# Performance work log

Hardware: AMD Instinct MI355X
Metric: run time of the kernel (lower is better)

## Reference

```python
import jax, jax.numpy as jnp
import numpy as np

B, N, H, KRATE = 128, 400, 128, 0.2
EPS = 1e-9


def setup_inputs() -> dict:
    key = jax.random.key(0)
    ks = jax.random.split(key, 16)
    # correlation-like input: symmetric, values in (-1,1), unit diagonal
    x = jax.random.normal(ks[0], (B, N, N), dtype=jnp.float32)
    x = jnp.tanh(0.3 * x)
    x = 0.5 * (x + x.transpose(0, 2, 1))
    eye = jnp.eye(N, dtype=jnp.float32)
    x = x * (1.0 - eye) + eye

    def lin(k, fan_in, shape):
        return jax.random.normal(k, shape, dtype=jnp.float32) / np.sqrt(fan_in).astype(np.float32)

    return {
        "x": x,
        "slength": jnp.full((B,), 100, dtype=jnp.int32),
        # AE denoiser (num_of_node=N, hidden=H)
        "enc1_w": lin(ks[1], N, (N, H)), "enc1_b": jnp.zeros((H,), jnp.float32),
        "enc2_w": lin(ks[2], N, (N, H)), "enc2_b": jnp.zeros((H,), jnp.float32),
        "dec2_w": lin(ks[3], H, (H, N)), "dec2_b": jnp.zeros((N,), jnp.float32),
        "dec1_w": lin(ks[4], H, (H, N)), "dec1_b": jnp.zeros((N,), jnp.float32),
        # GCN predictor
        "gcn1_w": lin(ks[5], N, (N, H)), "gcn1_b": jnp.zeros((H,), jnp.float32),
        "gcn2_w": lin(ks[6], H, (H, H)), "gcn2_b": jnp.zeros((H,), jnp.float32),
        # classification head Linear(128 -> 2)
        "fc_w": lin(ks[7], H, (H, 2)), "fc_b": jnp.zeros((2,), jnp.float32),
    }


def reference(x, slength, enc1_w, enc1_b, enc2_w, enc2_b, dec2_w, dec2_b,
              dec1_w, dec1_b, gcn1_w, gcn1_b, gcn2_w, gcn2_b, fc_w, fc_b):
    eye = jnp.eye(N, dtype=x.dtype)

    # fisher transform + normalize by [0,0] entry
    xf = 0.5 * jnp.log((1.0 + x + EPS) / (1.0 - x + EPS))
    xf = xf / xf[:, 0, 0][:, None, None]

    # --- DA / AE denoiser: deltax = AE(xf), symmetrized ---
    out1 = jax.nn.relu(jnp.einsum('bij,jh->bih', xf, enc1_w) + enc1_b).transpose(0, 2, 1)  # [B,H,N]
    out2 = jax.nn.relu(jnp.einsum('bhn,nk->bhk', out1, enc2_w) + enc2_b)                   # [B,H,H]
    out2 = jax.nn.relu(jnp.einsum('bhk,kn->bhn', out2, dec2_w) + dec2_b + out1)            # [B,H,N]
    out2 = out2.transpose(0, 2, 1)                                                         # [B,N,H]
    delta = jnp.einsum('bnh,hm->bnm', out2, dec1_w) + dec1_b                               # [B,N,N]
    delta = 0.5 * (delta + delta.transpose(0, 2, 1))
    x2 = xf + delta * (1.0 - eye)

    # --- predictor on detached x2 ---
    xp = jax.lax.stop_gradient(x2)

    # topk sparsification at rate 0.2 over flattened NxN per sample
    k = int(N * N * KRATE)
    flat = xp.reshape(B, N * N)
    _, idx = jax.lax.top_k(flat, k)
    mask = jnp.zeros((B, N * N), xp.dtype).at[jnp.arange(B)[:, None], idx].set(1.0)
    A = xp * mask.reshape(B, N, N)

    # GCN norm (PyG gcn_norm with add_remaining_self_loops, fill=1)
    diag = jnp.diagonal(A, axis1=1, axis2=2)
    A = A + eye[None] * jnp.where(diag == 0.0, 1.0, 0.0)[:, :, None]
    deg = A.sum(axis=1)                      # scatter of edge weight on col index
    dinv = deg ** -0.5
    dinv = jnp.where(jnp.isinf(dinv), 0.0, dinv)
    An = dinv[:, :, None] * A * dinv[:, None, :]  # An[b,i,j] = dinv[i]*A[i,j]*dinv[j]

    # GCNConv1 -> ReLU -> GCNConv2 (aggregate onto col/target index)
    h = jax.nn.relu(jnp.einsum('bij,bif->bjf', An, xp @ gcn1_w) + gcn1_b)  # [B,N,H]
    h = jnp.einsum('bij,bif->bjf', An, h @ gcn2_w) + gcn2_b                # [B,N,H]

    pooled = h.mean(axis=1)                  # mean over nodes -> [B,H]
    out = jax.nn.relu(pooled) @ fc_w + fc_b  # [B,2]
    return out
```

## Files before the change

### kernel.cpp

```cpp
#include <hip/hip_runtime.h>
#include <hip/hip_bf16.h>
#include <math.h>

#define BATCH 128
#define NNODE 400
#define HID   128
#define NN    (NNODE*NNODE)
#define KSEL  32000
#define EQCAP 1024
#define EPSF  1e-9f
#define TSPLIT 8
#define SEG   (NN / TSPLIT)
#define NT    7
#define KC400 14
#define FRAGS (KC400*4096)
#define PLA   57344

__device__ __forceinline__ unsigned tokey(float f) {
  unsigned u = __float_as_uint(f);
  return (u & 0x80000000u) ? ~u : (u | 0x80000000u);
}

__device__ __forceinline__ short f2bf(float f) {
  unsigned u = __float_as_uint(f);
  u += 0x7fffu + ((u >> 16) & 1u);
  return (short)(u >> 16);
}
__device__ __forceinline__ float bf2f(short s) {
  return __uint_as_float(((unsigned)(unsigned short)s) << 16);
}

__device__ __forceinline__ float xfhw(float xv, float cmul) {
  float la = __builtin_amdgcn_logf(1.0f + xv + EPSF);
  float lb = __builtin_amdgcn_logf(1.0f - xv + EPSF);
  return (la - lb) * cmul;
}

typedef __attribute__((ext_vector_type(8))) short s8v;
typedef __attribute__((ext_vector_type(4))) short s4v;
typedef __attribute__((ext_vector_type(4))) float f4v;

#define BK 16
#define LP 68

template<bool AT, bool BIAS, bool RES, bool RELU, bool TS>
__global__ void __launch_bounds__(256) gemm64(
    const float* __restrict__ A, long sA, int lda,
    const float* __restrict__ B, long sB, int ldb,
    const float* __restrict__ bias,
    const float* __restrict__ Res, long sRes,
    float* __restrict__ C, long sC, int ldc,
    int M, int Nc, int K)
{
  __shared__ float As[BK][LP];
  __shared__ float Bs[BK][LP];
  const int bz = blockIdx.z;
  A += (size_t)bz * sA;
  B += (size_t)bz * sB;
  C += (size_t)bz * sC;
  const float* Rp = RES ? (Res + (size_t)bz * sRes) : nullptr;

  const int n0 = blockIdx.x * 64;
  const int m0 = blockIdx.y * 64;
  const int tid = threadIdx.x;
  const int tx = tid & 15, ty = tid >> 4;
  const bool edgeM = (m0 + 64 > M);
  const bool edgeN = (n0 + 64 > Nc);

  float acc[4][4];
#pragma unroll
  for (int i = 0; i < 4; ++i)
#pragma unroll
    for (int j = 0; j < 4; ++j) acc[i][j] = 0.f;

  for (int k0 = 0; k0 < K; k0 += BK) {
    if (!AT) {
      const int m = tid & 63, g = tid >> 6;
      if (!edgeM) {
        const float4 v = *(const float4*)(A + (size_t)(m0 + m) * lda + k0 + 4 * g);
        As[4 * g + 0][m] = v.x; As[4 * g + 1][m] = v.y;
        As[4 * g + 2][m] = v.z; As[4 * g + 3][m] = v.w;
      } else {
        const int gm = m0 + m;
        const bool ok = gm < M;
#pragma unroll
        for (int j = 0; j < 4; ++j)
          As[4 * g + j][m] = ok ? A[(size_t)gm * lda + k0 + 4 * g + j] : 0.f;
      }
    } else {
      const int k = tid >> 4, mg = tid & 15;
      if (!edgeM) {
        const float4 v = *(const float4*)(A + (size_t)(k0 + k) * lda + m0 + 4 * mg);
        *(float4*)&As[k][4 * mg] = v;
      } else {
#pragma unroll
        for (int j = 0; j < 4; ++j) {
          const int gm = m0 + 4 * mg + j;
          As[k][4 * mg + j] = (gm < M) ? A[(size_t)(k0 + k) * lda + gm] : 0.f;
        }
      }
    }
    {
      const int k = tid >> 4, ng = tid & 15;
      if (!edgeN) {
        const float4 v = *(const float4*)(B + (size_t)(k0 + k) * ldb + n0 + 4 * ng);
        *(float4*)&Bs[k][4 * ng] = v;
      } else {
#pragma unroll
        for (int j = 0; j < 4; ++j) {
          const int gn = n0 + 4 * ng + j;
          Bs[k][4 * ng + j] = (gn < Nc) ? B[(size_t)(k0 + k) * ldb + gn] : 0.f;
        }
      }
    }
    __syncthreads();
#pragma unroll
    for (int kk = 0; kk < BK; ++kk) {
      const float4 a = *(const float4*)&As[kk][ty << 2];
      const float4 b = *(const float4*)&Bs[kk][tx << 2];
      const float av[4] = {a.x, a.y, a.z, a.w};
      const float bv[4] = {b.x, b.y, b.z, b.w};
#pragma unroll
      for (int i = 0; i < 4; ++i)
#pragma unroll
        for (int j = 0; j < 4; ++j) acc[i][j] += av[i] * bv[j];
    }
    __syncthreads();
  }

#pragma unroll
  for (int i = 0; i < 4; ++i) {
    const int m = m0 + (ty << 2) + i;
    if (m >= M) continue;
#pragma unroll
    for (int j = 0; j < 4; ++j) {
      const int n = n0 + (tx << 2) + j;
      if (n >= Nc) continue;
      float v = acc[i][j];
      if (BIAS) v += bias[n];
      const size_t loc = TS ? ((size_t)n * ldc + m) : ((size_t)m * ldc + n);
      if (RES) v += Rp[loc];
      if (RELU) v = fmaxf(v, 0.f);
      C[loc] = v;
    }
  }
}

__global__ void bsplit5(
    const float* __restrict__ gcn1_w, const float* __restrict__ gcn2_w,
    const float* __restrict__ enc1_w, const float* __restrict__ enc2_w,
    const float* __restrict__ dec1_w,
    short* __restrict__ w1frag, short* __restrict__ w2frag,
    short* __restrict__ e1frag, short* __restrict__ e2frag,
    short* __restrict__ dfrag) {
  const float* W; short* out; int K, Kpad, N, Npad;
  switch (blockIdx.y) {
    case 0: W = gcn1_w; out = w1frag; K = NNODE; Kpad = 448; N = HID;   Npad = 128; break;
    case 1: W = gcn2_w; out = w2frag; K = HID;   Kpad = 128; N = HID;   Npad = 128; break;
    case 2: W = enc1_w; out = e1frag; K = NNODE; Kpad = 448; N = HID;   Npad = 128; break;
    case 3: W = enc2_w; out = e2frag; K = NNODE; Kpad = 448; N = HID;   Npad = 128; break;
    default: W = dec1_w; out = dfrag; K = HID;   Kpad = 128; N = NNODE; Npad = 448; break;
  }
  int t = blockIdx.x * 256 + threadIdx.x;
  if (t >= Kpad * Npad) return;
  int k = t / Npad, n = t - k * Npad;
  float v = (k < K && n < N) ? W[(size_t)k * N + n] : 0.f;
  short hi = f2bf(v);
  short lo = f2bf(v - bf2f(hi));
  int ntiles = Npad >> 4;
  size_t idx = (((size_t)(k >> 5) * ntiles + (n >> 4)) * 64
                + (((k >> 3) & 3) * 16 + (n & 15))) * 8 + (k & 7);
  size_t PL = (size_t)(Kpad >> 5) * ntiles * 512;
  out[idx] = hi;
  out[PL + idx] = lo;
}

template<bool AT, bool FRAG, bool BIAS, bool RELU, bool SCL, bool TS, bool XF,
         bool MASK, bool DSCL>
__global__ void __launch_bounds__(256) mfgemm(
    const float* __restrict__ A, long sA, int lda,
    const short* __restrict__ Bf, long sB, int kc,
    const float* __restrict__ bias,
    const float* __restrict__ scl,
    float* __restrict__ Cf, long sCf, int ldc,
    short* __restrict__ Cfrag, long sCfrag, int okc,
    const float* __restrict__ denomp, float* __restrict__ xfout,
    const unsigned* __restrict__ taup, float* __restrict__ Aout,
    float* __restrict__ degp, int* __restrict__ eqcntp,
    int* __restrict__ eqidxp, const float* __restrict__ dsclp,
    int M, int K)
{
  __shared__ float As[64][68];
  __shared__ float cs[MASK ? NNODE : 1];
  const int bz = blockIdx.y;
  A += (size_t)bz * sA;
  Bf += (size_t)bz * sB;
  if (SCL) scl += (size_t)bz * NNODE;
  if (!FRAG) Cf += (size_t)bz * sCf;
  else       Cfrag += (size_t)bz * sCfrag;
  if (XF) xfout += (size_t)bz * sA;
  const float cmul = XF ? (0.34657359027997264f / denomp[bz]) : 0.f;
  const unsigned tk = MASK ? taup[bz] : 0u;
  if (MASK) { Aout += (size_t)bz * NN; degp += (size_t)bz * NNODE;
              eqcntp += bz; eqidxp += (size_t)bz * EQCAP; }
  if (DSCL) dsclp += (size_t)bz * NNODE;

  const int tid = threadIdx.x;
  const int lane = tid & 63, wave = tid >> 6;
  const int wqm = wave >> 1, wqn = wave & 1;
  const int quad = lane >> 4, l15 = lane & 15;
  const int m0 = blockIdx.x * 64;

  if (MASK) {
    for (int i = tid; i < NNODE; i += 256) cs[i] = 0.f;
    __syncthreads();
  }

  f4v acc[2][4];
#pragma unroll
  for (int i = 0; i < 2; ++i)
#pragma unroll
    for (int j = 0; j < 4; ++j) acc[i][j] = (f4v){0.f, 0.f, 0.f, 0.f};

  const int nstage = (K + 63) >> 6;
  for (int st = 0; st < nstage; ++st) {
    const int k0 = st << 6;
    if (st) __syncthreads();
    if (!AT) {
      const int mrow = tid >> 4;
      const int k4 = (tid & 15) << 2;
#pragma unroll
      for (int u = 0; u < 4; ++u) {
        const int m = mrow + (u << 4);
        const int gm = m0 + m, gk = k0 + k4;
        float4 v = {0.f, 0.f, 0.f, 0.f};
        if (gm < M) {
          if (gk + 4 <= K) {
            float4 xv = *(const float4*)(A + (size_t)gm * lda + gk);
            if (XF) {
              v.x = xfhw(xv.x, cmul);
              v.y = xfhw(xv.y, cmul);
              v.z = xfhw(xv.z, cmul);
              v.w = xfhw(xv.w, cmul);
              *(float4*)(xfout + (size_t)gm * lda + gk) = v;
            } else v = xv;
            if (MASK) {
              float4 av;
              float* pa = (float*)&av;
              const float* px = (const float*)&v;
#pragma unroll
              for (int j = 0; j < 4; ++j) {
                const unsigned key = tokey(px[j]);
                float a = (key > tk) ? px[j] : 0.f;
                if (key == tk) {
                  int p = atomicAdd(eqcntp, 1);
                  if (p < EQCAP) eqidxp[p] = gm * NNODE + gk + j;
                }
                if (a != 0.f) atomicAdd(&cs[gk + j], a);
                pa[j] = a;
              }
              *(float4*)(Aout + (size_t)gm * NNODE + gk) = av;
            }
          } else {
            float* pv = (float*)&v;
#pragma unroll
            for (int j = 0; j < 4; ++j)
              if (gk + j < K) {
                float xv = A[(size_t)gm * lda + gk + j];
                if (XF) {
                  pv[j] = xfhw(xv, cmul);
                  xfout[(size_t)gm * lda + gk + j] = pv[j];
                } else pv[j] = xv;
                if (MASK) {
                  const unsigned key = tokey(pv[j]);
                  float a = (key > tk) ? pv[j] : 0.f;
                  if (key == tk) {
                    int p = atomicAdd(eqcntp, 1);
                    if (p < EQCAP) eqidxp[p] = gm * NNODE + gk + j;
                  }
                  if (a != 0.f) atomicAdd(&cs[gk + j], a);
                  Aout[(size_t)gm * NNODE + gk + j] = a;
                }
              }
          }
        }
        *(float4*)&As[m][k4] = v;
      }
    } else {
      const int kk = tid >> 4;
      const int m4 = (tid & 15) << 2;
#pragma unroll
      for (int u = 0; u < 4; ++u) {
        const int gk = k0 + kk + (u << 4);
        float4 v = {0.f, 0.f, 0.f, 0.f};
        if (gk < K) {
          const float ds = DSCL ? dsclp[gk] : 1.f;
          if (m0 + m4 + 4 <= M) {
            v = *(const float4*)(A + (size_t)gk * lda + m0 + m4);
            if (DSCL) { v.x *= ds; v.y *= ds; v.z *= ds; v.w *= ds; }
          } else {
            float* pv = (float*)&v;
#pragma unroll
            for (int j = 0; j < 4; ++j)
              if (m0 + m4 + j < M) {
                float t = A[(size_t)gk * lda + m0 + m4 + j];
                pv[j] = DSCL ? t * ds : t;
              }
          }
        }
        As[m4 + 0][kk + (u << 4)] = v.x;
        As[m4 + 1][kk + (u << 4)] = v.y;
        As[m4 + 2][kk + (u << 4)] = v.z;
        As[m4 + 3][kk + (u << 4)] = v.w;
      }
    }
    __syncthreads();

#pragma unroll
    for (int c2 = 0; c2 < 2; ++c2) {
      const int c = (st << 1) + c2;
      s8v bhi[4], blo[4];
#pragma unroll
      for (int nt = 0; nt < 4; ++nt) {
        const int ntg = (wqn << 2) + nt;
        const size_t off = (((size_t)c * 8 + ntg) * 64 + lane) * 8;
        bhi[nt] = *(const s8v*)(Bf + off);
        blo[nt] = *(const s8v*)(Bf + (size_t)kc * 4096 + off);
      }
#pragma unroll
      for (int mt = 0; mt < 2; ++mt) {
        const int row = (wqm << 5) + (mt << 4) + l15;
        const int kof = (c2 << 5) + (quad << 3);
        const f4v a0 = *(const f4v*)&As[row][kof];
        const f4v a1 = *(const f4v*)&As[row][kof + 4];
        s8v ah, al;
#pragma unroll
        for (int j = 0; j < 4; ++j) {
          short h0 = f2bf(a0[j]); ah[j] = h0; al[j] = f2bf(a0[j] - bf2f(h0));
          short h1 = f2bf(a1[j]); ah[j + 4] = h1; al[j + 4] = f2bf(a1[j] - bf2f(h1));
        }
#pragma unroll
        for (int nt = 0; nt < 4; ++nt) {
          acc[mt][nt] = __builtin_amdgcn_mfma_f32_16x16x32_bf16(ah, bhi[nt], acc[mt][nt], 0, 0, 0);
          acc[mt][nt] = __builtin_amdgcn_mfma_f32_16x16x32_bf16(ah, blo[nt], acc[mt][nt], 0, 0, 0);
          acc[mt][nt] = __builtin_amdgcn_mfma_f32_16x16x32_bf16(al, bhi[nt], acc[mt][nt], 0, 0, 0);
        }
      }
    }
  }

  if (MASK) {
    __syncthreads();
    for (int j = tid; j < NNODE; j += 256) {
      const float s = cs[j];
      if (s != 0.f) atomicAdd(&degp[j], s);
    }
  }

  if (TS) {
    for (int nh = 0; nh < 2; ++nh) {
      __syncthreads();
      if (wqn == nh) {
#pragma unroll
        for (int mt = 0; mt < 2; ++mt)
#pragma unroll
          for (int nt = 0; nt < 4; ++nt) {
            const int tn = (nt << 4) + l15;
            const int n  = (wqn << 6) + tn;
            const int mc = (wqm << 5) + (mt << 4) + (quad << 2);
            const f4v a = acc[mt][nt];
#pragma unroll
            for (int reg = 0; reg < 4; ++reg) {
              float v = a[reg];
              if (SCL) v *= scl[m0 + mc + reg];
              if (BIAS) v += bias[n];
              if (RELU) v = fmaxf(v, 0.f);
              As[tn][mc + reg] = v;
            }
          }
      }
      __syncthreads();
      const int row = tid >> 2, cq = tid & 3;
#pragma unroll
      for (int u = 0; u < 4; ++u) {
        const int col = (cq + (u << 2)) << 2;
        if (m0 + col + 4 <= M) {
          const float4 v = *(const float4*)&As[row][col];
          *(float4*)(Cf + (size_t)((nh << 6) + row) * ldc + m0 + col) = v;
        }
      }
    }
    return;
  }

#pragma unroll
  for (int mt = 0; mt < 2; ++mt) {
    const int mb = m0 + (wqm << 5) + (mt << 4) + (quad << 2);
#pragma unroll
    for (int nt = 0; nt < 4; ++nt) {
      const int n = (wqn << 6) + (nt << 4) + l15;
      const f4v a = acc[mt][nt];
      if (!FRAG) {
#pragma unroll
        for (int reg = 0; reg < 4; ++reg) {
          const int m = mb + reg;
          if (m < M) {
            float v = a[reg];
            if (SCL) v *= scl[m];
            if (BIAS) v += bias[n];
            if (RELU) v = fmaxf(v, 0.f);
            Cf[(size_t)m * ldc + n] = v;
          }
        }
      } else {
        s4v h4, l4;
#pragma unroll
        for (int reg = 0; reg < 4; ++reg) {
          const int m = mb + reg;
          float v = (m < M) ? (SCL ? a[reg] * scl[m] : a[reg]) : 0.f;
          short hh = f2bf(v);
          h4[reg] = hh; l4[reg] = f2bf(v - bf2f(hh));
        }
        const int chunkT = mb >> 5, quadT = (mb >> 3) & 3, jT0 = mb & 7;
        const size_t off = (((size_t)chunkT * 8 + (wqn << 2) + nt) * 64
                            + quadT * 16 + l15) * 8 + jT0;
        *(s4v*)(Cfrag + off) = h4;
        *(s4v*)(Cfrag + (size_t)okc * 4096 + off) = l4;
      }
    }
  }
}

__global__ void __launch_bounds__(256) g4mf(
    const float* __restrict__ o1,
    const short* __restrict__ wfrag,
    const float* __restrict__ bias,
    float* __restrict__ xf,
    unsigned* __restrict__ ghist)
{
  __shared__ float D2[64][68];
  __shared__ unsigned hist[2048];
  const int b = blockIdx.y;
  int p = blockIdx.x, bi = 0;
  while (p >= NT - bi) { p -= NT - bi; ++bi; }
  const int bj = bi + p;
  const int I0 = bi * 64, J0 = bj * 64;
  const bool diag = (bi == bj);

  o1 += (size_t)b * HID * NNODE;
  xf += (size_t)b * NN;
  unsigned* gh = ghist + (size_t)b * 4096;

  const int tid = threadIdx.x;
  const int lane = tid & 63, wave = tid >> 6;
  const int wq = wave & 1;
  const bool d1 = wave < 2;
  const int Bt = (d1 ? bj : bi) * 4;
  const int quad = lane >> 4, l15 = lane & 15;
  const int M0 = d1 ? I0 : J0;

  for (int i = tid; i < 2048; i += 256) hist[i] = 0u;

  f4v acc[2][4];
#pragma unroll
  for (int i = 0; i < 2; ++i)
#pragma unroll
    for (int j = 0; j < 4; ++j) acc[i][j] = (f4v){0.f, 0.f, 0.f, 0.f};

  const int gm0 = M0 + (wq << 5) + l15;

  for (int c = 0; c < 4; ++c) {
    const int k0 = c << 5;
    s8v bhi[4], blo[4];
#pragma unroll
    for (int nt = 0; nt < 4; ++nt) {
      const int ntg = Bt + nt;
      const size_t off = (((size_t)c * 28 + ntg) * 64 + lane) * 8;
      bhi[nt] = *(const s8v*)(wfrag + off);
      blo[nt] = *(const s8v*)(wfrag + PLA + off);
    }
#pragma unroll
    for (int mt = 0; mt < 2; ++mt) {
      const int gm = gm0 + (mt << 4);
      float av[8];
      if (gm < NNODE) {
        const float* cp = o1 + (size_t)(k0 + (quad << 3)) * NNODE + gm;
#pragma unroll
        for (int j = 0; j < 8; ++j) av[j] = cp[(size_t)j * NNODE];
      } else {
#pragma unroll
        for (int j = 0; j < 8; ++j) av[j] = 0.f;
      }
      s8v ah, al;
#pragma unroll
      for (int j = 0; j < 8; ++j) {
        short h = f2bf(av[j]); ah[j] = h; al[j] = f2bf(av[j] - bf2f(h));
      }
#pragma unroll
      for (int nt = 0; nt < 4; ++nt) {
        acc[mt][nt] = __builtin_amdgcn_mfma_f32_16x16x32_bf16(ah, bhi[nt], acc[mt][nt], 0, 0, 0);
        acc[mt][nt] = __builtin_amdgcn_mfma_f32_16x16x32_bf16(ah, blo[nt], acc[mt][nt], 0, 0, 0);
        acc[mt][nt] = __builtin_amdgcn_mfma_f32_16x16x32_bf16(al, bhi[nt], acc[mt][nt], 0, 0, 0);
      }
    }
  }

  if (!d1) {
#pragma unroll
    for (int mt = 0; mt < 2; ++mt) {
      const int mb = (wq << 5) + (mt << 4) + (quad << 2);
#pragma unroll
      for (int nt = 0; nt < 4; ++nt) {
        const int nn = (nt << 4) + l15;
        const f4v a = acc[mt][nt];
#pragma unroll
        for (int reg = 0; reg < 4; ++reg) D2[mb + reg][nn] = a[reg];
      }
    }
  }
  __syncthreads();

  if (d1) {
    const unsigned w = diag ? 1u : 2u;
#pragma unroll
    for (int mt = 0; mt < 2; ++mt) {
      const int a0 = (wq << 5) + (mt << 4) + (quad << 2);
#pragma unroll
      for (int nt = 0; nt < 4; ++nt) {
        const int nn = (nt << 4) + l15;
        const int gj = J0 + nn;
        const f4v d1v = acc[mt][nt];
        const f4v d2t = *(const f4v*)&D2[nn][a0];
        f4v vv;
#pragma unroll
        for (int reg = 0; reg < 4; ++reg) {
          const int gi = I0 + a0 + reg;
          float v = 0.f;
          if (gi < NNODE && gj < NNODE) {
            v = xf[(size_t)gi * NNODE + gj];
            if (gi != gj)
              v += 0.5f * (d1v[reg] + d2t[reg] + bias[gj] + bias[gi]);
            const unsigned bin = tokey(v) >> 20;
            atomicAdd(&hist[bin >> 1], w << ((bin & 1) << 4));
          }
          vv[reg] = v;
        }
#pragma unroll
        for (int reg = 0; reg < 4; ++reg) {
          const int gi = I0 + a0 + reg;
          if (gi < NNODE && gj < NNODE) xf[(size_t)gi * NNODE + gj] = vv[reg];
        }
        if (!diag && gj < NNODE && (I0 + a0 + 4 <= NNODE)) {
          *(float4*)(xf + (size_t)gj * NNODE + I0 + a0) = *(float4*)&vv;
        }
      }
    }
  }
  __syncthreads();
  for (int i = tid; i < 2048; i += 256) {
    const unsigned v = hist[i];
    const unsigned lo = v & 0xFFFFu, hi = v >> 16;
    if (lo) atomicAdd(&gh[2 * i], lo);
    if (hi) atomicAdd(&gh[2 * i + 1], hi);
  }
}

__global__ void tzd(const float* __restrict__ x, unsigned* __restrict__ ghist,
                    unsigned* __restrict__ sprefix, int* __restrict__ sk,
                    int* __restrict__ eqcnt, float* __restrict__ deg,
                    float* __restrict__ denom, unsigned* __restrict__ ccnt2) {
  int t = blockIdx.x * 256 + threadIdx.x;
  if (t < BATCH * 4096) ghist[t] = 0u;
  if (t < BATCH) {
    sprefix[t] = 0u; sk[t] = KSEL; eqcnt[t] = 0;
    float v = x[(size_t)t * NN];
    denom[t] = 0.5f * logf((1.0f + v + EPSF) / (1.0f - v + EPSF));
  }
  if (t < BATCH * TSPLIT) ccnt2[t] = 0u;
  if (t < BATCH * NNODE) deg[t] = 0.f;
}

__global__ void __launch_bounds__(256) thistA(const float* __restrict__ x2,
                                              const unsigned* __restrict__ sprefix,
                                              unsigned* __restrict__ ghist,
                                              unsigned* __restrict__ cand,
                                              unsigned* __restrict__ ccnt2) {
  __shared__ unsigned h[4096];
  __shared__ unsigned lcnt;
  const int b  = blockIdx.y;
  const int sb = blockIdx.x;
  const int tid = threadIdx.x;
  for (int i = tid; i < 4096; i += 256) h[i] = 0u;
  if (tid == 0) lcnt = 0u;
  __syncthreads();

  const unsigned prefix = sprefix[b];
  unsigned* cb = cand + (size_t)b * NN + (size_t)sb * SEG;
  const float4* p4 = (const float4*)(x2 + (size_t)b * NN);
  const int i0 = sb * (SEG / 4), i1 = i0 + (SEG / 4);
  for (int i = i0 + tid; i < i1; i += 256) {
    float4 v = p4[i];
    unsigned kk[4] = {tokey(v.x), tokey(v.y), tokey(v.z), tokey(v.w)};
#pragma unroll
    for (int q = 0; q < 4; ++q) {
      const unsigned key = kk[q];
      if ((key & 0xFFF00000u) == prefix) {
        atomicAdd(&h[(key >> 8) & 4095u], 1u);
        const unsigned pos = atomicAdd(&lcnt, 1u);
        cb[pos] = key;
      }
    }
  }
  __syncthreads();
  for (int i = tid; i < 4096; i += 256) {
    unsigned s = h[i];
    if (s) atomicAdd(&ghist[(size_t)b * 4096 + i], s);
  }
  if (tid == 0) ccnt2[b * TSPLIT + sb] = lcnt;
}

template<int SH>
__global__ void __launch_bounds__(256) tpick12(unsigned* __restrict__ ghist,
                                               unsigned* __restrict__ sprefix,
                                               int* __restrict__ sk) {
  const int b = blockIdx.x;
  __shared__ unsigned h[4096];
  __shared__ unsigned csum[256];
  unsigned* gh = ghist + (size_t)b * 4096;
  unsigned local = 0;
#pragma unroll
  for (int u = 0; u < 16; ++u) {
    unsigned v = gh[threadIdx.x * 16 + u];
    h[threadIdx.x * 16 + u] = v;
    local += v;
  }
  csum[threadIdx.x] = local;
  __syncthreads();
  if (threadIdx.x == 0) {
    int k = sk[b];
    int bin = 0;
    for (int ch = 255; ch >= 0; --ch) {
      int S = (int)csum[ch];
      if (S >= k) {
        for (int bb = ch * 16 + 15; bb >= ch * 16; --bb) {
          int c = (int)h[bb];
          if (c >= k) { bin = bb; break; }
          k -= c;
        }
        break;
      }
      k -= S;
    }
    sprefix[b] = sprefix[b] | ((unsigned)bin << SH);
    sk[b] = k;
  }
#pragma unroll
  for (int u = 0; u < 16; ++u) gh[threadIdx.x * 16 + u] = 0u;
}

__global__ void __launch_bounds__(256) thistC(const unsigned* __restrict__ cand,
                                              const unsigned* __restrict__ ccnt2,
                                              const unsigned* __restrict__ sprefix,
                                              const int* __restrict__ sk,
                                              unsigned* __restrict__ tau,
                                              int* __restrict__ rrem) {
  __shared__ unsigned h[8][256];
  const int b = blockIdx.x;
  const int tid = threadIdx.x;
  for (int i = tid; i < 8 * 256; i += 256) ((unsigned*)h)[i] = 0u;
  __syncthreads();
  const unsigned prefix = sprefix[b];
  const int rep = tid & 7;
  for (int sb = 0; sb < TSPLIT; ++sb) {
    const unsigned n = ccnt2[b * TSPLIT + sb];
    const unsigned* cp = cand + (size_t)b * NN + (size_t)sb * SEG;
    for (unsigned i = tid; i < n; i += 256) {
      const unsigned key = cp[i];
      if ((key & 0xFFFFFF00u) == prefix) atomicAdd(&h[rep][key & 255u], 1u);
    }
  }
  __syncthreads();
  if (tid < 256) {
    const unsigned s = h[0][tid] + h[1][tid] + h[2][tid] + h[3][tid]
                     + h[4][tid] + h[5][tid] + h[6][tid] + h[7][tid];
    h[0][tid] = s;
  }
  __syncthreads();
  if (tid == 0) {
    int k = sk[b];
    unsigned byte = 0u;
    for (int bin = 255; bin >= 0; --bin) {
      int c = (int)h[0][bin];
      if (c >= k) { byte = (unsigned)bin; break; }
      k -= c;
    }
    tau[b] = prefix | byte;
    rrem[b] = k;
  }
}

__global__ void __launch_bounds__(256) eqdinv(
    float* __restrict__ A, const float* __restrict__ x2,
    float* __restrict__ deg, float* __restrict__ dinv,
    const int* __restrict__ eqcnt, const int* __restrict__ eqidx,
    const int* __restrict__ rrem) {
  const int b = blockIdx.x;
  int cnt = eqcnt[b]; if (cnt > EQCAP) cnt = EQCAP;
  const int r = rrem[b];
  for (int t = threadIdx.x; t < cnt; t += 256) {
    int idx = eqidx[b * EQCAP + t];
    int rank = 0;
    for (int u = 0; u < cnt; ++u) rank += (eqidx[b * EQCAP + u] < idx) ? 1 : 0;
    if (rank < r) {
      float v = x2[(size_t)b * NN + idx];
      A[(size_t)b * NN + idx] = v;
      atomicAdd(&deg[b * NNODE + idx % NNODE], v);
    }
  }
  __syncthreads();
  for (int j = threadIdx.x; j < NNODE; j += 256) {
    float d = deg[b * NNODE + j];
    size_t o = (size_t)b * NN + (size_t)j * NNODE + j;
    if (A[o] == 0.f) { A[o] = 1.0f; d += 1.0f; }
    dinv[b * NNODE + j] = (d == 0.f) ? 0.f : 1.0f / sqrtf(d);
  }
}

__global__ void head_k(const float* __restrict__ h2, const float* __restrict__ fc_w,
                       const float* __restrict__ fc_b, float* __restrict__ out) {
  int b = blockIdx.x;
  int f = threadIdx.x;
  float s = 0.f;
  const float* p = h2 + (size_t)b * NNODE * HID + f;
  for (int j = 0; j < NNODE; ++j) s += p[(size_t)j * HID];
  float pv = fmaxf(s / (float)NNODE, 0.f);
  __shared__ float r0[128], r1[128];
  r0[f] = pv * fc_w[f * 2 + 0];
  r1[f] = pv * fc_w[f * 2 + 1];
  __syncthreads();
  for (int sft = 64; sft > 0; sft >>= 1) {
    if (f < sft) { r0[f] += r0[f + sft]; r1[f] += r1[f + sft]; }
    __syncthreads();
  }
  if (f == 0) {
    out[b * 2 + 0] = r0[0] + fc_b[0];
    out[b * 2 + 1] = r1[0] + fc_b[1];
  }
}

extern "C" void kernel_launch(void* const* d_in, const int* in_sizes, int n_in,
                              void* d_out, int out_size, void* d_ws, size_t ws_size,
                              hipStream_t stream) {
  const float* x      = (const float*)d_in[0];
  const float* enc1_w = (const float*)d_in[2];
  const float* enc1_b = (const float*)d_in[3];
  const float* enc2_w = (const float*)d_in[4];
  const float* enc2_b = (const float*)d_in[5];
  const float* dec2_w = (const float*)d_in[6];
  const float* dec2_b = (const float*)d_in[7];
  const float* dec1_w = (const float*)d_in[8];
  const float* dec1_b = (const float*)d_in[9];
  const float* gcn1_w = (const float*)d_in[10];
  const float* gcn1_b = (const float*)d_in[11];
  const float* gcn2_w = (const float*)d_in[12];
  const float* gcn2_b = (const float*)d_in[13];
  const float* fc_w   = (const float*)d_in[14];
  const float* fc_b   = (const float*)d_in[15];
  float* out = (float*)d_out;
  (void)in_sizes; (void)n_in; (void)out_size; (void)ws_size;

  float* ws = (float*)d_ws;
  size_t off = 0;
  auto take = [&](size_t n) { float* p = ws + off; off += (n + 63) & ~(size_t)63; return p; };
  float* xf   = take((size_t)BATCH * NN);
  float* dl   = take((size_t)BATCH * NN);
  float* o1   = take((size_t)BATCH * HID * NNODE);
  float* o2   = take((size_t)BATCH * HID * HID);
  float* hbuf = take((size_t)BATCH * NNODE * HID);
  float* denom = take(BATCH);
  float* dinv  = take((size_t)BATCH * NNODE);
  float* deg   = take((size_t)BATCH * NNODE);
  unsigned* tau = (unsigned*)take(BATCH);
  int* rrem  = (int*)take(BATCH);
  int* eqcnt = (int*)take(BATCH);
  int* eqidx = (int*)take((size_t)BATCH * EQCAP);
  unsigned* ghist   = (unsigned*)take((size_t)BATCH * 4096);
  unsigned* sprefix = (unsigned*)take(BATCH);
  int*      sk      = (int*)take(BATCH);
  unsigned* ccnt2   = (unsigned*)take((size_t)BATCH * TSPLIT);
  short* w1frag = (short*)take((size_t)FRAGS + 64);
  short* w2frag = (short*)take((size_t)4 * 4096 + 64);
  short* e1frag = (short*)take((size_t)FRAGS + 64);
  short* e2frag = (short*)take((size_t)FRAGS + 64);
  short* dfrag  = (short*)take((size_t)PLA + 64);
  short* xwfrag = (short*)o1;
  unsigned* cand = (unsigned*)dl;
  const long sXW = 2L * FRAGS;

  tzd<<<2048, 256, 0, stream>>>(x, ghist, sprefix, sk, eqcnt, deg, denom, ccnt2);
  bsplit5<<<dim3(224, 5), 256, 0, stream>>>(gcn1_w, gcn2_w, enc1_w, enc2_w, dec1_w,
                                            w1frag, w2frag, e1frag, e2frag, dfrag);

  mfgemm<false, false, true, true, false, true, true, false, false><<<dim3(7, BATCH), 256, 0, stream>>>(
      x, NN, NNODE, e1frag, 0, KC400, enc1_b, nullptr,
      o1, (long)HID * NNODE, NNODE, nullptr, 0, 0, denom, xf,
      nullptr, nullptr, nullptr, nullptr, nullptr, nullptr, NNODE, NNODE);
  mfgemm<false, false, true, true, false, false, false, false, false><<<dim3(2, BATCH), 256, 0, stream>>>(
      o1, (long)HID * NNODE, NNODE, e2frag, 0, KC400, enc2_b, nullptr,
      o2, (long)HID * HID, HID, nullptr, 0, 0, nullptr, nullptr,
      nullptr, nullptr, nullptr, nullptr, nullptr, nullptr, HID, NNODE);
  gemm64<false, true, true, true, false><<<dim3(7, 2, BATCH), 256, 0, stream>>>(
      o2, (long)HID * HID, HID, dec2_w, 0, NNODE, dec2_b,
      o1, (long)HID * NNODE, o1, (long)HID * NNODE, NNODE, HID, NNODE, HID);

  g4mf<<<dim3(NT * (NT + 1) / 2, BATCH), 256, 0, stream>>>(o1, dfrag, dec1_b, xf, ghist);

  tpick12<20><<<BATCH, 256, 0, stream>>>(ghist, sprefix, sk);
  thistA<<<dim3(TSPLIT, BATCH), 256, 0, stream>>>(xf, sprefix, ghist, cand, ccnt2);
  tpick12<8><<<BATCH, 256, 0, stream>>>(ghist, sprefix, sk);
  thistC<<<BATCH, 256, 0, stream>>>(cand, ccnt2, sprefix, sk, tau, rrem);

  mfgemm<false, true, false, false, false, false, false, true, false><<<dim3(7, BATCH), 256, 0, stream>>>(
      xf, NN, NNODE, w1frag, 0, KC400, nullptr, nullptr,
      nullptr, 0, 128, xwfrag, sXW, KC400, nullptr, nullptr,
      tau, dl, deg, eqcnt, eqidx, nullptr, NNODE, NNODE);
  eqdinv<<<BATCH, 256, 0, stream>>>(dl, xf, deg, dinv, eqcnt, eqidx, rrem);

  mfgemm<true, false, true, true, true, false, false, false, true><<<dim3(7, BATCH), 256, 0, stream>>>(
      dl, NN, NNODE, xwfrag, sXW, KC400, gcn1_b, dinv,
      hbuf, (long)NNODE * HID, HID, nullptr, 0, 0, nullptr, nullptr,
      nullptr, nullptr, nullptr, nullptr, nullptr, dinv, NNODE, NNODE);
  mfgemm<false, true, false, false, false, false, false, false, false><<<dim3(7, BATCH), 256, 0, stream>>>(
      hbuf, (long)NNODE * HID, HID, w2frag, 0, 4, nullptr, nullptr,
      nullptr, 0, 128, xwfrag, sXW, KC400, nullptr, nullptr,
      nullptr, nullptr, nullptr, nullptr, nullptr, nullptr, NNODE, HID);
  mfgemm<true, false, true, false, true, false, false, false, true><<<dim3(7, BATCH), 256, 0, stream>>>(
      dl, NN, NNODE, xwfrag, sXW, KC400, gcn2_b, dinv,
      hbuf, (long)NNODE * HID, HID, nullptr, 0, 0, nullptr, nullptr,
      nullptr, nullptr, nullptr, nullptr, nullptr, dinv, NNODE, NNODE);

  head_k<<<BATCH, HID, 0, stream>>>(hbuf, fc_w, fc_b, out);
}
```

Baseline: 634.9 us.

## Fuse mean-pool into last GCN GEMM and merge threshold pick into thistC

```diff
diff --git a/kernel.cpp b/kernel.cpp
--- a/kernel.cpp
+++ b/kernel.cpp
@@ -176,7 +176,7 @@
 }
 
 template<bool AT, bool FRAG, bool BIAS, bool RELU, bool SCL, bool TS, bool XF,
-         bool MASK, bool DSCL>
+         bool MASK, bool DSCL, bool POOL>
 __global__ void __launch_bounds__(256) mfgemm(
     const float* __restrict__ A, long sA, int lda,
     const short* __restrict__ Bf, long sB, int kc,
@@ -188,10 +188,12 @@
     const unsigned* __restrict__ taup, float* __restrict__ Aout,
     float* __restrict__ degp, int* __restrict__ eqcntp,
     int* __restrict__ eqidxp, const float* __restrict__ dsclp,
+    float* __restrict__ poolp,
     int M, int K)
 {
   __shared__ float As[64][68];
   __shared__ float cs[MASK ? NNODE : 1];
+  __shared__ float ps[POOL ? HID : 1];
   const int bz = blockIdx.y;
   A += (size_t)bz * sA;
   Bf += (size_t)bz * sB;
@@ -204,6 +206,7 @@
   if (MASK) { Aout += (size_t)bz * NN; degp += (size_t)bz * NNODE;
               eqcntp += bz; eqidxp += (size_t)bz * EQCAP; }
   if (DSCL) dsclp += (size_t)bz * NNODE;
+  if (POOL) poolp += (size_t)bz * HID;
 
   const int tid = threadIdx.x;
   const int lane = tid & 63, wave = tid >> 6;
@@ -214,6 +217,9 @@
   if (MASK) {
     for (int i = tid; i < NNODE; i += 256) cs[i] = 0.f;
     __syncthreads();
+  }
+  if (POOL) {
+    for (int i = tid; i < HID; i += 256) ps[i] = 0.f;
   }
 
   f4v acc[2][4];
@@ -357,6 +363,37 @@
     }
   }
 
+  if (POOL) {
+    __syncthreads();
+#pragma unroll
+    for (int nt = 0; nt < 4; ++nt) {
+      const int n = (wqn << 6) + (nt << 4) + l15;
+      float s = 0.f;
+#pragma unroll
+      for (int mt = 0; mt < 2; ++mt) {
+        const int mb = m0 + (wqm << 5) + (mt << 4) + (quad << 2);
+        const f4v a = acc[mt][nt];
+#pragma unroll
+        for (int reg = 0; reg < 4; ++reg) {
+          const int m = mb + reg;
+          if (m < M) {
+            float v = a[reg];
+            if (SCL) v *= scl[m];
+            if (BIAS) v += bias[n];
+            s += v;
+          }
+        }
+      }
+      atomicAdd(&ps[n], s);
+    }
+    __syncthreads();
+    for (int i = tid; i < HID; i += 256) {
+      const float s = ps[i];
+      if (s != 0.f) atomicAdd(&poolp[i], s);
+    }
+    return;
+  }
+
   if (TS) {
     for (int nh = 0; nh < 2; ++nh) {
       __syncthreads();
@@ -568,7 +605,8 @@
 __global__ void tzd(const float* __restrict__ x, unsigned* __restrict__ ghist,
                     unsigned* __restrict__ sprefix, int* __restrict__ sk,
                     int* __restrict__ eqcnt, float* __restrict__ deg,
-                    float* __restrict__ denom, unsigned* __restrict__ ccnt2) {
+                    float* __restrict__ denom, unsigned* __restrict__ ccnt2,
+                    float* __restrict__ pooled) {
   int t = blockIdx.x * 256 + threadIdx.x;
   if (t < BATCH * 4096) ghist[t] = 0u;
   if (t < BATCH) {
@@ -578,6 +616,7 @@
   }
   if (t < BATCH * TSPLIT) ccnt2[t] = 0u;
   if (t < BATCH * NNODE) deg[t] = 0.f;
+  if (t < BATCH * HID) pooled[t] = 0.f;
 }
 
 __global__ void __launch_bounds__(256) thistA(const float* __restrict__ x2,
@@ -658,39 +697,72 @@
   for (int u = 0; u < 16; ++u) gh[threadIdx.x * 16 + u] = 0u;
 }
 
-__global__ void __launch_bounds__(256) thistC(const unsigned* __restrict__ cand,
+__global__ void __launch_bounds__(256) thistC(const unsigned* __restrict__ ghist,
+                                              const unsigned* __restrict__ cand,
                                               const unsigned* __restrict__ ccnt2,
                                               const unsigned* __restrict__ sprefix,
                                               const int* __restrict__ sk,
                                               unsigned* __restrict__ tau,
                                               int* __restrict__ rrem) {
-  __shared__ unsigned h[8][256];
+  __shared__ unsigned h12[4096];
+  __shared__ unsigned csum[256];
+  __shared__ unsigned h8[8][256];
+  __shared__ unsigned spfx;
+  __shared__ int skk;
   const int b = blockIdx.x;
   const int tid = threadIdx.x;
-  for (int i = tid; i < 8 * 256; i += 256) ((unsigned*)h)[i] = 0u;
-  __syncthreads();
-  const unsigned prefix = sprefix[b];
+  const unsigned* gh = ghist + (size_t)b * 4096;
+  unsigned local = 0;
+#pragma unroll
+  for (int u = 0; u < 16; ++u) {
+    unsigned v = gh[tid * 16 + u];
+    h12[tid * 16 + u] = v;
+    local += v;
+  }
+  csum[tid] = local;
+  for (int i = tid; i < 8 * 256; i += 256) ((unsigned*)h8)[i] = 0u;
+  __syncthreads();
+  if (tid == 0) {
+    int k = sk[b];
+    int bin = 0;
+    for (int ch = 255; ch >= 0; --ch) {
+      int S = (int)csum[ch];
+      if (S >= k) {
+        for (int bb = ch * 16 + 15; bb >= ch * 16; --bb) {
+          int c = (int)h12[bb];
+          if (c >= k) { bin = bb; break; }
+          k -= c;
+        }
+        break;
+      }
+      k -= S;
+    }
+    spfx = sprefix[b] | ((unsigned)bin << 8);
+    skk = k;
+  }
+  __syncthreads();
+  const unsigned prefix = spfx;
   const int rep = tid & 7;
   for (int sb = 0; sb < TSPLIT; ++sb) {
     const unsigned n = ccnt2[b * TSPLIT + sb];
     const unsigned* cp = cand + (size_t)b * NN + (size_t)sb * SEG;
     for (unsigned i = tid; i < n; i += 256) {
       const unsigned key = cp[i];
-      if ((key & 0xFFFFFF00u) == prefix) atomicAdd(&h[rep][key & 255u], 1u);
+      if ((key & 0xFFFFFF00u) == prefix) atomicAdd(&h8[rep][key & 255u], 1u);
     }
   }
   __syncthreads();
   if (tid < 256) {
-    const unsigned s = h[0][tid] + h[1][tid] + h[2][tid] + h[3][tid]
-                     + h[4][tid] + h[5][tid] + h[6][tid] + h[7][tid];
-    h[0][tid] = s;
+    const unsigned s = h8[0][tid] + h8[1][tid] + h8[2][tid] + h8[3][tid]
+                     + h8[4][tid] + h8[5][tid] + h8[6][tid] + h8[7][tid];
+    h8[0][tid] = s;
   }
   __syncthreads();
   if (tid == 0) {
-    int k = sk[b];
+    int k = skk;
     unsigned byte = 0u;
     for (int bin = 255; bin >= 0; --bin) {
-      int c = (int)h[0][bin];
+      int c = (int)h8[0][bin];
       if (c >= k) { byte = (unsigned)bin; break; }
       k -= c;
     }
@@ -726,14 +798,11 @@
   }
 }
 
-__global__ void head_k(const float* __restrict__ h2, const float* __restrict__ fc_w,
+__global__ void head_k(const float* __restrict__ pooled, const float* __restrict__ fc_w,
                        const float* __restrict__ fc_b, float* __restrict__ out) {
   int b = blockIdx.x;
   int f = threadIdx.x;
-  float s = 0.f;
-  const float* p = h2 + (size_t)b * NNODE * HID + f;
-  for (int j = 0; j < NNODE; ++j) s += p[(size_t)j * HID];
-  float pv = fmaxf(s / (float)NNODE, 0.f);
+  float pv = fmaxf(pooled[(size_t)b * HID + f] / (float)NNODE, 0.f);
   __shared__ float r0[128], r1[128];
   r0[f] = pv * fc_w[f * 2 + 0];
   r1[f] = pv * fc_w[f * 2 + 1];
@@ -780,6 +849,7 @@
   float* denom = take(BATCH);
   float* dinv  = take((size_t)BATCH * NNODE);
   float* deg   = take((size_t)BATCH * NNODE);
+  float* pooled = take((size_t)BATCH * HID);
   unsigned* tau = (unsigned*)take(BATCH);
   int* rrem  = (int*)take(BATCH);
   int* eqcnt = (int*)take(BATCH);
@@ -797,18 +867,18 @@
   unsigned* cand = (unsigned*)dl;
   const long sXW = 2L * FRAGS;
 
-  tzd<<<2048, 256, 0, stream>>>(x, ghist, sprefix, sk, eqcnt, deg, denom, ccnt2);
+  tzd<<<2048, 256, 0, stream>>>(x, ghist, sprefix, sk, eqcnt, deg, denom, ccnt2, pooled);
   bsplit5<<<dim3(224, 5), 256, 0, stream>>>(gcn1_w, gcn2_w, enc1_w, enc2_w, dec1_w,
                                             w1frag, w2frag, e1frag, e2frag, dfrag);
 
-  mfgemm<false, false, true, true, false, true, true, false, false><<<dim3(7, BATCH), 256, 0, stream>>>(
+  mfgemm<false, false, true, true, false, true, true, false, false, false><<<dim3(7, BATCH), 256, 0, stream>>>(
       x, NN, NNODE, e1frag, 0, KC400, enc1_b, nullptr,
       o1, (long)HID * NNODE, NNODE, nullptr, 0, 0, denom, xf,
-      nullptr, nullptr, nullptr, nullptr, nullptr, nullptr, NNODE, NNODE);
-  mfgemm<false, false, true, true, false, false, false, false, false><<<dim3(2, BATCH), 256, 0, stream>>>(
+      nullptr, nullptr, nullptr, nullptr, nullptr, nullptr, nullptr, NNODE, NNODE);
+  mfgemm<false, false, true, true, false, false, false, false, false, false><<<dim3(2, BATCH), 256, 0, stream>>>(
       o1, (long)HID * NNODE, NNODE, e2frag, 0, KC400, enc2_b, nullptr,
       o2, (long)HID * HID, HID, nullptr, 0, 0, nullptr, nullptr,
-      nullptr, nullptr, nullptr, nullptr, nullptr, nullptr, HID, NNODE);
+      nullptr, nullptr, nullptr, nullptr, nullptr, nullptr, nullptr, HID, NNODE);
   gemm64<false, true, true, true, false><<<dim3(7, 2, BATCH), 256, 0, stream>>>(
       o2, (long)HID * HID, HID, dec2_w, 0, NNODE, dec2_b,
       o1, (long)HID * NNODE, o1, (long)HID * NNODE, NNODE, HID, NNODE, HID);
@@ -817,27 +887,26 @@
 
   tpick12<20><<<BATCH, 256, 0, stream>>>(ghist, sprefix, sk);
   thistA<<<dim3(TSPLIT, BATCH), 256, 0, stream>>>(xf, sprefix, ghist, cand, ccnt2);
-  tpick12<8><<<BATCH, 256, 0, stream>>>(ghist, sprefix, sk);
-  thistC<<<BATCH, 256, 0, stream>>>(cand, ccnt2, sprefix, sk, tau, rrem);
-
-  mfgemm<false, true, false, false, false, false, false, true, false><<<dim3(7, BATCH), 256, 0, stream>>>(
+  thistC<<<BATCH, 256, 0, stream>>>(ghist, cand, ccnt2, sprefix, sk, tau, rrem);
+
+  mfgemm<false, true, false, false, false, false, false, true, false, false><<<dim3(7, BATCH), 256, 0, stream>>>(
       xf, NN, NNODE, w1frag, 0, KC400, nullptr, nullptr,
       nullptr, 0, 128, xwfrag, sXW, KC400, nullptr, nullptr,
-      tau, dl, deg, eqcnt, eqidx, nullptr, NNODE, NNODE);
+      tau, dl, deg, eqcnt, eqidx, nullptr, nullptr, NNODE, NNODE);
   eqdinv<<<BATCH, 256, 0, stream>>>(dl, xf, deg, dinv, eqcnt, eqidx, rrem);
 
-  mfgemm<true, false, true, true, true, false, false, false, true><<<dim3(7, BATCH), 256, 0, stream>>>(
+  mfgemm<true, false, true, true, true, false, false, false, true, false><<<dim3(7, BATCH), 256, 0, stream>>>(
       dl, NN, NNODE, xwfrag, sXW, KC400, gcn1_b, dinv,
       hbuf, (long)NNODE * HID, HID, nullptr, 0, 0, nullptr, nullptr,
-      nullptr, nullptr, nullptr, nullptr, nullptr, dinv, NNODE, NNODE);
-  mfgemm<false, true, false, false, false, false, false, false, false><<<dim3(7, BATCH), 256, 0, stream>>>(
+      nullptr, nullptr, nullptr, nullptr, nullptr, dinv, nullptr, NNODE, NNODE);
+  mfgemm<false, true, false, false, false, false, false, false, false, false><<<dim3(7, BATCH), 256, 0, stream>>>(
       hbuf, (long)NNODE * HID, HID, w2frag, 0, 4, nullptr, nullptr,
       nullptr, 0, 128, xwfrag, sXW, KC400, nullptr, nullptr,
-      nullptr, nullptr, nullptr, nullptr, nullptr, nullptr, NNODE, HID);
-  mfgemm<true, false, true, false, true, false, false, false, true><<<dim3(7, BATCH), 256, 0, stream>>>(
+      nullptr, nullptr, nullptr, nullptr, nullptr, nullptr, nullptr, NNODE, HID);
+  mfgemm<true, false, true, false, true, false, false, false, true, true><<<dim3(7, BATCH), 256, 0, stream>>>(
       dl, NN, NNODE, xwfrag, sXW, KC400, gcn2_b, dinv,
-      hbuf, (long)NNODE * HID, HID, nullptr, 0, 0, nullptr, nullptr,
-      nullptr, nullptr, nullptr, nullptr, nullptr, dinv, NNODE, NNODE);
-
-  head_k<<<BATCH, HID, 0, stream>>>(hbuf, fc_w, fc_b, out);
-}
+      nullptr, 0, HID, nullptr, 0, 0, nullptr, nullptr,
+      nullptr, nullptr, nullptr, nullptr, nullptr, dinv, pooled, NNODE, NNODE);
+
+  head_k<<<BATCH, HID, 0, stream>>>(pooled, fc_w, fc_b, out);
+}
```

Measured after the change: 622.3 us. 2.0% less time.
